# Optimization experiments

Hardware: AMD Instinct MI355X
Metric: run time of the kernel (lower is better)

Reference implementation:

```python
import jax, jax.numpy as jnp
import numpy as np

NEG = -1e9  # max-semiring 'zero' / structural mask value


def _cky_max(pot, lengths):
    """Max-plus CKY inside pass (torch_struct CKY_CRF with MaxSemiring).

    pot: [B, N, N] label-maxed span potentials, pot[b, i, j] = score of span (i, j).
    Returns [B] best binary-tree score for each sequence of given length.
    betaA[b, i, w]      = best score of span starting at i with width w (span [i, i+w]).
    betaB[b, j, N-1-w]  = best score of span ending at j with width w.
    """
    B, N, _ = pot.shape
    term = jnp.diagonal(pot, axis1=1, axis2=2)  # [B, N] width-0 spans
    betaA = jnp.full((B, N, N), NEG, dtype=pot.dtype).at[:, :, 0].set(term)
    betaB = jnp.full((B, N, N), NEG, dtype=pot.dtype).at[:, :, N - 1].set(term)
    for w in range(1, N):
        Y = betaA[:, : N - w, :w]       # [B, N-w, w] left children, widths 0..w-1
        Z = betaB[:, w:, N - w:]        # [B, N-w, w] right children (matching splits)
        span = jnp.diagonal(pot, offset=w, axis1=1, axis2=2)  # [B, N-w] pot[b, i, i+w]
        new = jnp.max(Y + Z, axis=-1) + span
        betaA = betaA.at[:, : N - w, w].set(new)
        betaB = betaB.at[:, w:, N - w - 1].set(new)
    final = betaA[:, 0, :]  # [B, N]: final[b, l-1] = best tree over [0, l-1]
    return final[jnp.arange(B), lengths - 1]


def setup_inputs() -> dict:
    key = jax.random.key(0)
    k1, k2 = jax.random.split(key)
    B, N, L = 64, 128, 32
    logits = jax.random.normal(k1, (B, N, N, L), dtype=jnp.float32)
    labels = jax.random.randint(k2, (B, N, N), 0, L, dtype=jnp.int64)
    return {"logits": logits, "labels": labels}


def reference(logits, labels):
    B, N, _, L = logits.shape
    gold_event = jax.nn.one_hot(jnp.maximum(labels, 0), L, dtype=logits.dtype)
    logits = logits - logits[..., :1]
    lengths = jnp.sum(labels[:, 0, :] != -100, axis=-1)
    augment = 1.0 - gold_event
    # force_root_constituent=True: forbid non-constituent root span
    augment = augment.at[jnp.arange(B), 0, lengths - 1, 0].add(-1e9)
    pot = jnp.max(logits + augment, axis=-1)  # max-semiring sum over label dim
    pred_score = _cky_max(pot, lengths)                      # [B]
    gold_score = jnp.sum(logits * gold_event, axis=(1, 2, 3))  # [B]
    margin_losses = jax.nn.relu(pred_score - gold_score)
    return jnp.mean(margin_losses)
```

## Files before the change

kernel.cpp:

```cpp
#include <hip/hip_runtime.h>

#define BATCH 64
#define SEQ   128
#define NLAB  32
#define NEGF  -3.0e38f
#define PA    132

__device__ __forceinline__ void bar_k(int K) {
    switch (K) {
    case 0: asm volatile("s_waitcnt lgkmcnt(0)" ::: "memory"); break;
    case 1: asm volatile("s_waitcnt lgkmcnt(1)" ::: "memory"); break;
    case 2: asm volatile("s_waitcnt lgkmcnt(2)" ::: "memory"); break;
    case 3: asm volatile("s_waitcnt lgkmcnt(3)" ::: "memory"); break;
    case 4: asm volatile("s_waitcnt lgkmcnt(4)" ::: "memory"); break;
    case 5: asm volatile("s_waitcnt lgkmcnt(5)" ::: "memory"); break;
    case 6: asm volatile("s_waitcnt lgkmcnt(6)" ::: "memory"); break;
    default: asm volatile("s_waitcnt lgkmcnt(7)" ::: "memory"); break;
    }
    __builtin_amdgcn_s_barrier();
}

__device__ __forceinline__ float qmax1(float v) {
    int t = __builtin_amdgcn_update_dpp(0, __float_as_int(v), 0xB1, 0xF, 0xF, true);
    return fmaxf(v, __int_as_float(t));
}
__device__ __forceinline__ float qmax2(float v) {
    int t = __builtin_amdgcn_update_dpp(0, __float_as_int(v), 0x4E, 0xF, 0xF, true);
    return fmaxf(v, __int_as_float(t));
}

__global__ __launch_bounds__(256) void pot_gold_kernel(
    const float* __restrict__ logits, const int* __restrict__ labels,
    float* __restrict__ pot, float* __restrict__ gpart, float* __restrict__ out)
{
    const int tid = threadIdx.x;
    const int wave = tid >> 6, lane = tid & 63;
    __shared__ __align__(16) float LP[4 * 16 * 36];
    __shared__ float gred[4];
    __shared__ int s_len;
    float* W = LP + wave * (16 * 36);

    const int block_cell0 = blockIdx.x * 256;
    const int b = block_cell0 >> 14;
    const bool has_row0 = (blockIdx.x & 63) == 0;

    if (blockIdx.x == 0 && tid == 0) out[0] = 0.0f;

    if (has_row0 && tid < 64) {
        const size_t base = (size_t)b << 14;
        int cnt = (labels[base + tid] != -100) + (labels[base + 64 + tid] != -100);
        #pragma unroll
        for (int d = 32; d; d >>= 1) cnt += __shfl_down(cnt, d, 64);
        if (tid == 0) s_len = cnt;
    }
    __syncthreads();
    const int len = has_row0 ? s_len : -1;

    float gacc = 0.0f;
    const int wave_cell0 = block_cell0 + wave * 64;

    #pragma unroll
    for (int chunk = 0; chunk < 4; ++chunk) {
        const int c0 = wave_cell0 + chunk * 16;
        const float4* src = reinterpret_cast<const float4*>(logits) + ((size_t)c0 << 3);
        const float4 f0 = src[lane];
        const float4 f1 = src[lane + 64];
        const int lv = (lane < 16) ? labels[c0 + lane] : 0;

        {
            const int cA = lane >> 3, tA = lane & 7;
            *reinterpret_cast<float4*>(W + cA * 36 + tA * 4) = f0;
            const int q1 = lane + 64;
            const int cB = q1 >> 3, tB = q1 & 7;
            *reinterpret_cast<float4*>(W + cB * 36 + tB * 4) = f1;
        }
        const int c = lane >> 2, u = lane & 3;
        const float4 r0 = *reinterpret_cast<const float4*>(W + c * 36 + u * 8);
        const float4 r1 = *reinterpret_cast<const float4*>(W + c * 36 + u * 8 + 4);

        int lab = __shfl(lv, c, 64);
        if (lab < 0) lab = 0;
        const float l0 = __shfl(r0.x, c << 2, 64);

        const int cell = c0 + c;
        const int ci = (cell >> 7) & (SEQ - 1);
        const int cj = cell & (SEQ - 1);
        const bool special = (ci == 0) && (cj == len - 1);

        const float vv[8] = { r0.x, r0.y, r0.z, r0.w, r1.x, r1.y, r1.z, r1.w };
        float m = NEGF, g = 0.0f;
        #pragma unroll
        for (int e = 0; e < 8; ++e) {
            const int l = u * 8 + e;
            const float r = vv[e] - l0;
            const bool isg = (l == lab);
            g = isg ? r : g;
            float cand = r + (isg ? 0.0f : 1.0f);
            if (l == 0 && special) cand -= 1.0e9f;
            m = fmaxf(m, cand);
        }
        m = fmaxf(m, __shfl_xor(m, 1, 64));
        m = fmaxf(m, __shfl_xor(m, 2, 64));
        g += __shfl_xor(g, 1, 64);
        g += __shfl_xor(g, 2, 64);
        if (u == 0) {
            pot[cell] = m;
            gacc += g;
        }
    }

    #pragma unroll
    for (int d = 1; d < 64; d <<= 1) gacc += __shfl_xor(gacc, d, 64);
    if (lane == 0) gred[wave] = gacc;
    __syncthreads();
    if (tid == 0)
        gpart[blockIdx.x] = gred[0] + gred[1] + gred[2] + gred[3];
}

__global__ __launch_bounds__(512, 1) void cky_kernel(
    const float* __restrict__ pot, const float* __restrict__ gpart,
    const int* __restrict__ labels, float* __restrict__ out)
{
    const int b = blockIdx.x;
    const int tid = threadIdx.x;
    const float* p = pot + (size_t)b * SEQ * SEQ;

    __shared__ __align__(16) float A[SEQ * PA];
    __shared__ __align__(16) float Bt[SEQ * PA];
    __shared__ int s_len;
    __shared__ float s_gold;

    if (tid < 64) {
        const size_t base = (size_t)b << 14;
        int cnt = (labels[base + tid] != -100) + (labels[base + 64 + tid] != -100);
        #pragma unroll
        for (int d = 32; d; d >>= 1) cnt += __shfl_down(cnt, d, 64);
        if (tid == 0) s_len = cnt;
    } else if (tid < 128) {
        float g = gpart[b * 64 + (tid - 64)];
        #pragma unroll
        for (int d = 32; d; d >>= 1) g += __shfl_down(g, d, 64);
        if (tid == 64) s_gold = g;
    }

    {
        const float4* p4 = reinterpret_cast<const float4*>(p);
        float4 vb[8];
        #pragma unroll
        for (int t = 0; t < 8; ++t) vb[t] = p4[tid + 512 * t];
        #pragma unroll
        for (int t = 0; t < 8; ++t) {
            const int qi = tid + 512 * t;
            const int i0 = qi >> 5;
            const int j0 = (qi & 31) << 2;
            const float vv[4] = { vb[t].x, vb[t].y, vb[t].z, vb[t].w };
            #pragma unroll
            for (int c2 = 0; c2 < 4; ++c2) {
                const int j = j0 + c2;
                if (j >= i0) {
                    A[i0 * PA + (j - i0)] = vv[c2];
                    Bt[j * PA + (SEQ - 1 - (j - i0))] = vv[c2];
                }
            }
        }
    }
    __syncthreads();

    const int i = tid >> 2, s = tid & 3;
    float alo[16], av[16], pv[16], md[16];
    float boq[4], bfq[4];

#define C0_BODY(Sv)                                                           \
    if (s == (Sv)) {                                                          \
        _Pragma("unroll")                                                     \
        for (int e = 0; e < 4; ++e) {                                         \
            const int m = 4 * (Sv) + e;                                       \
            if (m < d) {                                                      \
                const float bv = ((Sv) == ((d - 1) >> 2))                     \
                    ? ((e == 0) ? fq.w : (e == 1) ? fq.z : (e == 2) ? fq.y : fq.x) \
                    : boq[e];                                                 \
                part = fmaxf(part, av[d - 1 - m] + bv);                       \
            }                                                                 \
        }                                                                     \
    }

#define CH_BODY(Sv)                                                           \
    if (s == (Sv)) {                                                          \
        _Pragma("unroll")                                                     \
        for (int e = 0; e < 4; ++e) {                                         \
            const int m = 4 * (Sv) + e;                                       \
            if (m < d) {                                                      \
                part = fmaxf(part, av[d - 1 - m] + boq[e]);                   \
                const float bv = ((Sv) == ((d - 1) >> 2))                     \
                    ? ((e == 0) ? fq.w : (e == 1) ? fq.z : (e == 2) ? fq.y : fq.x) \
                    : bfq[e];                                                 \
                part = fmaxf(part, alo[d - 1 - m] + bv);                      \
            }                                                                 \
        }                                                                     \
    }

    #pragma unroll
    for (int t = 0; t < 4; ++t) {
        const float4 v = *reinterpret_cast<const float4*>(&A[i * PA + 4 * t]);
        pv[4*t] = v.x; pv[4*t+1] = v.y; pv[4*t+2] = v.z; pv[4*t+3] = v.w;
    }
    av[0] = pv[0];

    {
        const int jp = (i + 1 < SEQ) ? (i + 1) : (SEQ - 1);
        const float4 bv = *reinterpret_cast<const float4*>(&Bt[jp * PA + 124 - 4 * s]);
        boq[0] = bv.w; boq[1] = bv.z; boq[2] = bv.y; boq[3] = bv.x;
    }

    #pragma unroll
    for (int d = 1; d < 16; ++d) {
        const int j = i + d;
        const int jr = (j < SEQ) ? j : SEQ - 1;
        const float4 fq = *reinterpret_cast<const float4*>(&Bt[jr * PA + 124 - 4 * ((d - 1) >> 2)]);
        float part = NEGF;
        C0_BODY(0)
        C0_BODY(1)
        C0_BODY(2)
        C0_BODY(3)
        part = qmax2(qmax1(part));
        const float val = part + pv[d];
        av[d] = val;
        if (j < SEQ && s < 2) {
            float* pw = (s == 0) ? &A[i * PA + d] : &Bt[j * PA + (SEQ - 1 - d)];
            *pw = val;
        }
        __builtin_amdgcn_sched_barrier(0);
        if (d < 15) {
            const int jp = (j + 1 < SEQ) ? (j + 1) : (SEQ - 1);
            const float4 bv = *reinterpret_cast<const float4*>(&Bt[jp * PA + 124 - 4 * s]);
            boq[0] = bv.w; boq[1] = bv.z; boq[2] = bv.y; boq[3] = bv.x;
            bar_k(1);
        } else {
            bar_k(0);
        }
    }
    #pragma unroll
    for (int k = 0; k < 16; ++k) alo[k] = av[k];

    for (int W = 16; W < SEQ; W += 16) {
        #pragma unroll
        for (int t = 0; t < 4; ++t) {
            const float4 v = *reinterpret_cast<const float4*>(&A[i * PA + W + 4 * t]);
            pv[4*t] = v.x; pv[4*t+1] = v.y; pv[4*t+2] = v.z; pv[4*t+3] = v.w;
        }
        #pragma unroll
        for (int d = 0; d < 16; ++d) md[d] = NEGF;

        {
            const int k0 = s << 2;
            const float4 a = *reinterpret_cast<const float4*>(&A[i * PA + k0]);
            const float aa[4] = { a.x, a.y, a.z, a.w };
            #pragma unroll
            for (int d = 0; d < 16; ++d) {
                const int j = i + W + d;
                if (j < SEQ) {
                    const float* bp = &Bt[j * PA + (SEQ - W - d) + k0];
                    float b0, b1, b2, b3;
                    if ((d & 3) == 0) {
                        const float4 v = *reinterpret_cast<const float4*>(bp);
                        b0 = v.x; b1 = v.y; b2 = v.z; b3 = v.w;
                    } else if ((d & 3) == 2) {
                        const float2 v0 = *reinterpret_cast<const float2*>(bp);
                        const float2 v1 = *reinterpret_cast<const float2*>(bp + 2);
                        b0 = v0.x; b1 = v0.y; b2 = v1.x; b3 = v1.y;
                    } else {
                        b0 = bp[0];
                        const float2 v = *reinterpret_cast<const float2*>(bp + 1);
                        b1 = v.x; b2 = v.y; b3 = bp[3];
                    }
                    const float a0 = (k0 + 0 >= d) ? aa[0] : NEGF;
                    const float a1 = (k0 + 1 >= d) ? aa[1] : NEGF;
                    const float a2 = (k0 + 2 >= d) ? aa[2] : NEGF;
                    const float a3 = (k0 + 3 >= d) ? aa[3] : NEGF;
                    md[d] = fmaxf(md[d], fmaxf(fmaxf(a0 + b0, a1 + b1),
                                               fmaxf(a2 + b2, a3 + b3)));
                }
            }
        }
        for (int q = s + 4; q < (W >> 2); q += 4) {
            const int k0 = q << 2;
            const float4 a = *reinterpret_cast<const float4*>(&A[i * PA + k0]);
            #pragma unroll
            for (int d = 0; d < 16; ++d) {
                const int j = i + W + d;
                if (j < SEQ) {
                    const float* bp = &Bt[j * PA + (SEQ - W - d) + k0];
                    float b0, b1, b2, b3;
                    if ((d & 3) == 0) {
                        const float4 v = *reinterpret_cast<const float4*>(bp);
                        b0 = v.x; b1 = v.y; b2 = v.z; b3 = v.w;
                    } else if ((d & 3) == 2) {
                        const float2 v0 = *reinterpret_cast<const float2*>(bp);
                        const float2 v1 = *reinterpret_cast<const float2*>(bp + 2);
                        b0 = v0.x; b1 = v0.y; b2 = v1.x; b3 = v1.y;
                    } else {
                        b0 = bp[0];
                        const float2 v = *reinterpret_cast<const float2*>(bp + 1);
                        b1 = v.x; b2 = v.y; b3 = bp[3];
                    }
                    md[d] = fmaxf(md[d], fmaxf(fmaxf(a.x + b0, a.y + b1),
                                               fmaxf(a.z + b2, a.w + b3)));
                }
            }
        }
        #pragma unroll
        for (int d = 0; d < 16; ++d) {
            md[d] = qmax2(qmax1(md[d]));
        }

        {
            const int j = i + W;
            const float val = md[0] + pv[0];
            av[0] = val;
            if (j < SEQ && s < 2) {
                float* pw = (s == 0) ? &A[i * PA + W] : &Bt[j * PA + (SEQ - 1 - W)];
                *pw = val;
            }
            __builtin_amdgcn_sched_barrier(0);
            const int jp = (j + 1 < SEQ) ? (j + 1) : (SEQ - 1);
            const float4 bv = *reinterpret_cast<const float4*>(&Bt[jp * PA + 124 - 4 * s]);
            const float4 fv = *reinterpret_cast<const float4*>(&Bt[jp * PA + 124 - W - 4 * s]);
            boq[0] = bv.w; boq[1] = bv.z; boq[2] = bv.y; boq[3] = bv.x;
            bfq[0] = fv.w; bfq[1] = fv.z; bfq[2] = fv.y; bfq[3] = fv.x;
            bar_k(2);
        }
        #pragma unroll
        for (int d = 1; d < 16; ++d) {
            const int w = W + d;
            const int j = i + w;
            const int jr = (j < SEQ) ? j : SEQ - 1;
            const float4 fq = *reinterpret_cast<const float4*>(
                &Bt[jr * PA + 124 - W - 4 * ((d - 1) >> 2)]);
            float part = NEGF;
            CH_BODY(0)
            CH_BODY(1)
            CH_BODY(2)
            CH_BODY(3)
            part = qmax2(qmax1(part));
            const float val = fmaxf(part, md[d]) + pv[d];
            av[d] = val;
            if (j < SEQ && s < 2) {
                float* pw = (s == 0) ? &A[i * PA + w] : &Bt[j * PA + (SEQ - 1 - w)];
                *pw = val;
            }
            __builtin_amdgcn_sched_barrier(0);
            if (d < 15) {
                const int jp = (j + 1 < SEQ) ? (j + 1) : (SEQ - 1);
                const float4 bv = *reinterpret_cast<const float4*>(&Bt[jp * PA + 124 - 4 * s]);
                const float4 fv = *reinterpret_cast<const float4*>(&Bt[jp * PA + 124 - W - 4 * s]);
                boq[0] = bv.w; boq[1] = bv.z; boq[2] = bv.y; boq[3] = bv.x;
                bfq[0] = fv.w; bfq[1] = fv.z; bfq[2] = fv.y; bfq[3] = fv.x;
                bar_k(2);
            } else {
                bar_k(0);
            }
        }
    }

    if (tid == 0) {
        const int len = s_len;
        const float pred = A[len - 1];
        const float margin = fmaxf(pred - s_gold, 0.0f);
        atomicAdd(out, margin * (1.0f / (float)BATCH));
    }
#undef C0_BODY
#undef CH_BODY
}

extern "C" void kernel_launch(void* const* d_in, const int* in_sizes, int n_in,
                              void* d_out, int out_size, void* d_ws, size_t ws_size,
                              hipStream_t stream) {
    const float* logits = (const float*)d_in[0];
    const int* labels = (const int*)d_in[1];
    float* out = (float*)d_out;

    float* pot = (float*)d_ws;
    float* gpart = pot + (size_t)BATCH * SEQ * SEQ;

    pot_gold_kernel<<<BATCH * SEQ * SEQ / 256, 256, 0, stream>>>(
        logits, labels, pot, gpart, out);
    cky_kernel<<<BATCH, 512, 0, stream>>>(pot, gpart, labels, out);
}
```

Baseline: 256.5 us.

## Register-tile CKY bulk split reduction over 4 rows with 16-lane cooperation

Restructures the bulk (far-split) part of each 16-wide CKY block so a 16-lane group computes a 4-row by 16-width register tile. It reads left children from A and the right-child windows from A rows, realigned with lane-dependent selects, reduces across lanes with row-level DPP, and shares results through a shared staging buffer plus a block barrier. Pot values are now read directly from global memory instead of being preloaded into LDS, and LDS is NEG-initialised up front. The aim is to raise arithmetic reuse per LDS load in the dominant O(N^3) part, at the cost of an extra __syncthreads per block, more registers and wasted work on masked lanes.

```diff
diff --git a/kernel.cpp b/kernel.cpp
--- a/kernel.cpp
+++ b/kernel.cpp
@@ -11,11 +11,7 @@
     case 0: asm volatile("s_waitcnt lgkmcnt(0)" ::: "memory"); break;
     case 1: asm volatile("s_waitcnt lgkmcnt(1)" ::: "memory"); break;
     case 2: asm volatile("s_waitcnt lgkmcnt(2)" ::: "memory"); break;
-    case 3: asm volatile("s_waitcnt lgkmcnt(3)" ::: "memory"); break;
-    case 4: asm volatile("s_waitcnt lgkmcnt(4)" ::: "memory"); break;
-    case 5: asm volatile("s_waitcnt lgkmcnt(5)" ::: "memory"); break;
-    case 6: asm volatile("s_waitcnt lgkmcnt(6)" ::: "memory"); break;
-    default: asm volatile("s_waitcnt lgkmcnt(7)" ::: "memory"); break;
+    default: asm volatile("s_waitcnt lgkmcnt(4)" ::: "memory"); break;
     }
     __builtin_amdgcn_s_barrier();
 }
@@ -26,6 +22,14 @@
 }
 __device__ __forceinline__ float qmax2(float v) {
     int t = __builtin_amdgcn_update_dpp(0, __float_as_int(v), 0x4E, 0xF, 0xF, true);
+    return fmaxf(v, __int_as_float(t));
+}
+__device__ __forceinline__ float rmax4(float v) {
+    int t = __builtin_amdgcn_update_dpp(0, __float_as_int(v), 0x124, 0xF, 0xF, true);
+    return fmaxf(v, __int_as_float(t));
+}
+__device__ __forceinline__ float rmax8(float v) {
+    int t = __builtin_amdgcn_update_dpp(0, __float_as_int(v), 0x128, 0xF, 0xF, true);
     return fmaxf(v, __int_as_float(t));
 }
 
@@ -125,49 +129,48 @@
     const int tid = threadIdx.x;
     const float* p = pot + (size_t)b * SEQ * SEQ;
 
-    __shared__ __align__(16) float A[SEQ * PA];
-    __shared__ __align__(16) float Bt[SEQ * PA];
+    __shared__ __align__(16) float SH[4 + 2 * SEQ * PA + SEQ * 20];
+    float* A = SH + 4;
+    float* Bt = A + SEQ * PA;
+    float* stage = Bt + SEQ * PA;
     __shared__ int s_len;
     __shared__ float s_gold;
 
-    if (tid < 64) {
+    {
+        const float4 nf = { NEGF, NEGF, NEGF, NEGF };
+        float4* sh4 = reinterpret_cast<float4*>(SH);
+        const int NQ4 = (4 + 2 * SEQ * PA + SEQ * 20) / 4;
+        for (int q = tid; q < NQ4; q += 512) sh4[q] = nf;
+    }
+    __syncthreads();
+
+    if (tid < 128) {
+        const float v = p[tid * 129];
+        A[tid * PA] = v;
+        Bt[tid * PA + (SEQ - 1)] = v;
+    } else if (tid < 192) {
+        const int lane = tid - 128;
         const size_t base = (size_t)b << 14;
-        int cnt = (labels[base + tid] != -100) + (labels[base + 64 + tid] != -100);
+        int cnt = (labels[base + lane] != -100) + (labels[base + 64 + lane] != -100);
         #pragma unroll
         for (int d = 32; d; d >>= 1) cnt += __shfl_down(cnt, d, 64);
-        if (tid == 0) s_len = cnt;
-    } else if (tid < 128) {
-        float g = gpart[b * 64 + (tid - 64)];
+        if (lane == 0) s_len = cnt;
+    } else if (tid < 256) {
+        const int lane = tid - 192;
+        float g = gpart[b * 64 + lane];
         #pragma unroll
         for (int d = 32; d; d >>= 1) g += __shfl_down(g, d, 64);
-        if (tid == 64) s_gold = g;
-    }
-
-    {
-        const float4* p4 = reinterpret_cast<const float4*>(p);
-        float4 vb[8];
-        #pragma unroll
-        for (int t = 0; t < 8; ++t) vb[t] = p4[tid + 512 * t];
-        #pragma unroll
-        for (int t = 0; t < 8; ++t) {
-            const int qi = tid + 512 * t;
-            const int i0 = qi >> 5;
-            const int j0 = (qi & 31) << 2;
-            const float vv[4] = { vb[t].x, vb[t].y, vb[t].z, vb[t].w };
-            #pragma unroll
-            for (int c2 = 0; c2 < 4; ++c2) {
-                const int j = j0 + c2;
-                if (j >= i0) {
-                    A[i0 * PA + (j - i0)] = vv[c2];
-                    Bt[j * PA + (SEQ - 1 - (j - i0))] = vv[c2];
-                }
-            }
-        }
+        if (lane == 0) s_gold = g;
     }
     __syncthreads();
 
     const int i = tid >> 2, s = tid & 3;
-    float alo[16], av[16], pv[16], md[16];
+    const int g  = tid >> 4;
+    const int i0 = g << 2;
+    const int sp = tid & 15;
+    const int rot = (4 - (sp & 3)) & 3;
+
+    float alo[16], av[16];
     float boq[4], bfq[4];
 
 #define C0_BODY(Sv)                                                           \
@@ -199,12 +202,13 @@
         }                                                                     \
     }
 
-    #pragma unroll
-    for (int t = 0; t < 4; ++t) {
-        const float4 v = *reinterpret_cast<const float4*>(&A[i * PA + 4 * t]);
-        pv[4*t] = v.x; pv[4*t+1] = v.y; pv[4*t+2] = v.z; pv[4*t+3] = v.w;
-    }
-    av[0] = pv[0];
+    float pvc[16];
+    {
+        const float* prow = p + i * 129;
+        #pragma unroll
+        for (int k = 0; k < 16; ++k) pvc[k] = prow[k];
+    }
+    av[0] = pvc[0];
 
     {
         const int jp = (i + 1 < SEQ) ? (i + 1) : (SEQ - 1);
@@ -223,7 +227,7 @@
         C0_BODY(2)
         C0_BODY(3)
         part = qmax2(qmax1(part));
-        const float val = part + pv[d];
+        const float val = part + pvc[d];
         av[d] = val;
         if (j < SEQ && s < 2) {
             float* pw = (s == 0) ? &A[i * PA + d] : &Bt[j * PA + (SEQ - 1 - d)];
@@ -243,79 +247,92 @@
     for (int k = 0; k < 16; ++k) alo[k] = av[k];
 
     for (int W = 16; W < SEQ; W += 16) {
-        #pragma unroll
-        for (int t = 0; t < 4; ++t) {
-            const float4 v = *reinterpret_cast<const float4*>(&A[i * PA + W + 4 * t]);
-            pv[4*t] = v.x; pv[4*t+1] = v.y; pv[4*t+2] = v.z; pv[4*t+3] = v.w;
-        }
-        #pragma unroll
-        for (int d = 0; d < 16; ++d) md[d] = NEGF;
-
+        float pvn[16];
         {
-            const int k0 = s << 2;
-            const float4 a = *reinterpret_cast<const float4*>(&A[i * PA + k0]);
-            const float aa[4] = { a.x, a.y, a.z, a.w };
+            const float* prow = p + i * 129 + W;
             #pragma unroll
-            for (int d = 0; d < 16; ++d) {
-                const int j = i + W + d;
-                if (j < SEQ) {
-                    const float* bp = &Bt[j * PA + (SEQ - W - d) + k0];
-                    float b0, b1, b2, b3;
-                    if ((d & 3) == 0) {
-                        const float4 v = *reinterpret_cast<const float4*>(bp);
-                        b0 = v.x; b1 = v.y; b2 = v.z; b3 = v.w;
-                    } else if ((d & 3) == 2) {
-                        const float2 v0 = *reinterpret_cast<const float2*>(bp);
-                        const float2 v1 = *reinterpret_cast<const float2*>(bp + 2);
-                        b0 = v0.x; b1 = v0.y; b2 = v1.x; b3 = v1.y;
-                    } else {
-                        b0 = bp[0];
-                        const float2 v = *reinterpret_cast<const float2*>(bp + 1);
-                        b1 = v.x; b2 = v.y; b3 = bp[3];
+            for (int k = 0; k < 16; ++k) pvn[k] = prow[k];
+        }
+
+        if (i0 + W <= 127) {
+            float md2[4][16];
+            #pragma unroll
+            for (int r = 0; r < 4; ++r)
+                #pragma unroll
+                for (int d = 0; d < 16; ++d) md2[r][d] = NEGF;
+
+            const int NIT = (W + 64) >> 6;
+            for (int n = 0; n < NIT; ++n) {
+                #pragma unroll
+                for (int ep = 0; ep < 4; ++ep) {
+                    const int pbase = (n << 6) + (ep << 4);
+                    if (pbase <= W) {
+                        const int pp = pbase + sp;
+                        const bool act = (pp <= W);
+                        float avv[4];
+                        #pragma unroll
+                        for (int r = 0; r < 4; ++r) {
+                            const float v = A[(i0 + r) * PA + (pp - 1 - r)];
+                            avv[r] = act ? v : NEGF;
+                        }
+                        const int prow_ = (i0 + pp <= 127) ? (i0 + pp) : 127;
+                        int al = (W - pp) & ~3; if (al < 0) al = 0;
+                        const float* wp = &A[prow_ * PA + al];
+                        float w24[24];
+                        #pragma unroll
+                        for (int t = 0; t < 6; ++t) {
+                            const float4 v = *reinterpret_cast<const float4*>(wp + 4 * t);
+                            w24[4*t] = v.x; w24[4*t+1] = v.y; w24[4*t+2] = v.z; w24[4*t+3] = v.w;
+                        }
+                        float wr[19];
+                        {
+                            float t1[21];
+                            #pragma unroll
+                            for (int k = 0; k < 21; ++k) t1[k] = (rot & 1) ? w24[k + 1] : w24[k];
+                            #pragma unroll
+                            for (int k = 0; k < 19; ++k) wr[k] = (rot & 2) ? t1[k + 2] : t1[k];
+                        }
+                        #pragma unroll
+                        for (int r = 0; r < 4; ++r)
+                            #pragma unroll
+                            for (int d = 0; d < 16; ++d)
+                                md2[r][d] = fmaxf(md2[r][d], avv[r] + wr[r + d]);
                     }
-                    const float a0 = (k0 + 0 >= d) ? aa[0] : NEGF;
-                    const float a1 = (k0 + 1 >= d) ? aa[1] : NEGF;
-                    const float a2 = (k0 + 2 >= d) ? aa[2] : NEGF;
-                    const float a3 = (k0 + 3 >= d) ? aa[3] : NEGF;
-                    md[d] = fmaxf(md[d], fmaxf(fmaxf(a0 + b0, a1 + b1),
-                                               fmaxf(a2 + b2, a3 + b3)));
                 }
             }
-        }
-        for (int q = s + 4; q < (W >> 2); q += 4) {
-            const int k0 = q << 2;
-            const float4 a = *reinterpret_cast<const float4*>(&A[i * PA + k0]);
             #pragma unroll
-            for (int d = 0; d < 16; ++d) {
-                const int j = i + W + d;
-                if (j < SEQ) {
-                    const float* bp = &Bt[j * PA + (SEQ - W - d) + k0];
-                    float b0, b1, b2, b3;
-                    if ((d & 3) == 0) {
-                        const float4 v = *reinterpret_cast<const float4*>(bp);
-                        b0 = v.x; b1 = v.y; b2 = v.z; b3 = v.w;
-                    } else if ((d & 3) == 2) {
-                        const float2 v0 = *reinterpret_cast<const float2*>(bp);
-                        const float2 v1 = *reinterpret_cast<const float2*>(bp + 2);
-                        b0 = v0.x; b1 = v0.y; b2 = v1.x; b3 = v1.y;
-                    } else {
-                        b0 = bp[0];
-                        const float2 v = *reinterpret_cast<const float2*>(bp + 1);
-                        b1 = v.x; b2 = v.y; b3 = bp[3];
+            for (int r = 0; r < 4; ++r)
+                #pragma unroll
+                for (int d = 0; d < 16; ++d) {
+                    float v = md2[r][d];
+                    v = qmax2(qmax1(v));
+                    v = rmax4(rmax8(v));
+                    md2[r][d] = v;
+                }
+            if (sp == 0) {
+                #pragma unroll
+                for (int r = 0; r < 4; ++r)
+                    #pragma unroll
+                    for (int t = 0; t < 4; ++t) {
+                        float4 v;
+                        v.x = md2[r][4*t]; v.y = md2[r][4*t+1];
+                        v.z = md2[r][4*t+2]; v.w = md2[r][4*t+3];
+                        *reinterpret_cast<float4*>(&stage[(i0 + r) * 20 + 4 * t]) = v;
                     }
-                    md[d] = fmaxf(md[d], fmaxf(fmaxf(a.x + b0, a.y + b1),
-                                               fmaxf(a.z + b2, a.w + b3)));
-                }
             }
         }
-        #pragma unroll
-        for (int d = 0; d < 16; ++d) {
-            md[d] = qmax2(qmax1(md[d]));
+        __syncthreads();
+
+        float mdv[16];
+        #pragma unroll
+        for (int t = 0; t < 4; ++t) {
+            const float4 v = *reinterpret_cast<const float4*>(&stage[i * 20 + 4 * t]);
+            mdv[4*t] = v.x; mdv[4*t+1] = v.y; mdv[4*t+2] = v.z; mdv[4*t+3] = v.w;
         }
 
         {
             const int j = i + W;
-            const float val = md[0] + pv[0];
+            const float val = mdv[0] + pvn[0];
             av[0] = val;
             if (j < SEQ && s < 2) {
                 float* pw = (s == 0) ? &A[i * PA + W] : &Bt[j * PA + (SEQ - 1 - W)];
@@ -342,7 +359,7 @@
             CH_BODY(2)
             CH_BODY(3)
             part = qmax2(qmax1(part));
-            const float val = fmaxf(part, md[d]) + pv[d];
+            const float val = fmaxf(part, mdv[d]) + pvn[d];
             av[d] = val;
             if (j < SEQ && s < 2) {
                 float* pw = (s == 0) ? &A[i * PA + w] : &Bt[j * PA + (SEQ - 1 - w)];
```

New measurement: 317.3 us. 23.7% more time.
